# Optimization experiments

Hardware: AMD Instinct MI355X
Metric: run time of the kernel (lower is better)

Reference implementation:

```python
import jax, jax.numpy as jnp
import numpy as np
from jax import lax

RATIOS = jnp.array([0.5, 1.0, 2.0], dtype=jnp.float32)
SCALES = jnp.array([8.0, 16.0, 32.0], dtype=jnp.float32)
IOU_THR = 0.5
BATCH_SIZE = 32            # module-level constant in the source
POS_RATIO = 1.0 / 3.0      # positive_ratio in the source


def _generate_anchors(fh, fw, ih, iw):
    """Vectorized version of RPN.generate_anchors. Returns (A,4) x1y1x2y2 anchors
    and an (A,) inside-image mask (static shapes; mask replaces boolean filtering)."""
    xs = iw / fw
    ys = ih / fh
    xc = (jnp.arange(fw, dtype=jnp.float32) + 0.5) * xs
    yc = (jnp.arange(fh, dtype=jnp.float32) + 0.5) * ys
    gx, gy = jnp.meshgrid(xc, yc, indexing='ij')
    centers = jnp.stack([gx.ravel(), gy.ravel()], axis=1)          # (fh*fw, 2)
    h = jnp.sqrt(SCALES[None, :] ** 2 / RATIOS[:, None]) * ys       # (3,3)
    w = h * RATIOS[:, None] * xs / ys
    wh = jnp.stack([w.ravel(), h.ravel()], axis=1)                  # (9, 2)
    lo = centers[:, None, :] - wh[None, :, :] / 2
    hi = centers[:, None, :] + wh[None, :, :] / 2
    anchors = jnp.concatenate([lo, hi], axis=2).reshape(-1, 4)      # (A, 4)
    inside = ((anchors[:, 0] >= 0) & (anchors[:, 1] >= 0) &
              (anchors[:, 2] <= iw) & (anchors[:, 3] <= ih))
    return anchors, inside


def _iou_matrix(anchors, gts):
    """Pairwise IoU between (A,4) and (G,4) corner boxes -> (A,G). Vectorizes the
    nested python loop in the original."""
    x1 = jnp.maximum(anchors[:, None, 0], gts[None, :, 0])
    y1 = jnp.maximum(anchors[:, None, 1], gts[None, :, 1])
    x2 = jnp.minimum(anchors[:, None, 2], gts[None, :, 2])
    y2 = jnp.minimum(anchors[:, None, 3], gts[None, :, 3])
    inter = jnp.maximum(x2 - x1, 0.0) * jnp.maximum(y2 - y1, 0.0)
    area_a = (anchors[:, 2] - anchors[:, 0]) * (anchors[:, 3] - anchors[:, 1])
    area_g = (gts[:, 2] - gts[:, 0]) * (gts[:, 3] - gts[:, 1])
    union = area_a[:, None] + area_g[None, :] - inter
    return jnp.where(inter > 0, inter / union, 0.0)


def _conv(x, w, b):
    return lax.conv_general_dilated(x, w, (1, 1), 'SAME',
                                    dimension_numbers=('NHWC', 'HWIO', 'NHWC')) + b


def setup_inputs() -> dict:
    key = jax.random.key(0)
    ks = jax.random.split(key, 11)
    B, H, W, C = 8, 64, 64, 512
    IMG = 1024
    std = 0.05  # keras RandomNormal default stddev
    features = jax.random.normal(ks[0], (B, H, W, C), jnp.float32)
    # 8 rows of boxes; rows 2..7 are the object boxes used by the RPN (x1,y1,x2,y2)
    xy = jax.random.uniform(ks[1], (8, 2), jnp.float32) * (IMG * 0.7)
    wh = jax.random.uniform(ks[2], (8, 2), jnp.float32) * (IMG * 0.2) + 16.0
    ground_truths = jnp.concatenate([xy, xy + wh], axis=1)
    return {
        'features': features,
        'ground_truths': ground_truths,
        'conv1_w': jax.random.normal(ks[3], (3, 3, C, 512), jnp.float32) * std,
        'conv1_b': jnp.zeros((512,), jnp.float32),
        'reg_w': jax.random.normal(ks[4], (1, 1, 512, 72), jnp.float32) * std,
        'reg_b': jnp.zeros((72,), jnp.float32),
        'cls_w': jax.random.normal(ks[5], (1, 1, 512, 9), jnp.float32) * std,
        'cls_b': jnp.zeros((9,), jnp.float32),
        'lmk_w': jax.random.normal(ks[6], (1, 1, 512, 54), jnp.float32) * std,
        'lmk_b': jnp.zeros((54,), jnp.float32),
        'img_h': IMG,
        'img_w': IMG,
    }


def reference(features, ground_truths, conv1_w, conv1_b, reg_w, reg_b,
              cls_w, cls_b, lmk_w, lmk_b, img_h, img_w):
    B, H, W, C = features.shape
    anchors, inside = _generate_anchors(H, W, float(img_h), float(img_w))
    A = anchors.shape[0]
    gts = ground_truths[2:]                                   # (6,4)
    ious = _iou_matrix(anchors, gts)                          # (A,6)
    ious = jnp.where(inside[:, None], ious, -1.0)             # outside anchors never match

    best_iou = ious.max(axis=1)
    best_idx = ious.argmax(axis=1)
    gt_best = ious.max(axis=0)
    is_best = ((ious == gt_best[None, :]) & (gt_best[None, :] > -1.0)).any(axis=1)
    labels = jnp.where((best_iou >= IOU_THR) | is_best, 1, 0)
    labels = jnp.where(inside, labels, -1)

    # balanced subsampling (np.random.choice in the original -> rank-of-random trick)
    num_pos = int(POS_RATIO * BATCH_SIZE)
    num_neg = BATCH_SIZE - num_pos
    r = jax.random.uniform(jax.random.key(42), (A,), jnp.float32)

    def keep(mask, n):
        kv = jnp.where(mask, r, jnp.inf)
        order = jnp.argsort(kv)
        rank = jnp.zeros(A, jnp.int32).at[order].set(jnp.arange(A, dtype=jnp.int32))
        return mask & (rank < n)

    pos = keep(labels == 1, num_pos)
    neg = keep(labels == 0, num_neg)
    labels = jnp.where(pos, 1, jnp.where(neg, 0, -1)).astype(jnp.float32)

    eps = jnp.finfo(jnp.float32).eps
    wa = jnp.maximum(anchors[:, 2] - anchors[:, 0], eps)
    ha = jnp.maximum(anchors[:, 3] - anchors[:, 1], eps)
    xa = anchors[:, 0] + wa / 2
    ya = anchors[:, 1] + ha / 2
    mg = gts[best_idx]                                        # (A,4) matched gt
    wg = mg[:, 2] - mg[:, 0]
    hg = mg[:, 3] - mg[:, 1]
    xg = mg[:, 0] + wg / 2
    yg = mg[:, 1] + hg / 2
    deltas = jnp.stack([(xg - xa) / wa, (yg - ya) / ha,
                        jnp.log(wg / wa), jnp.log(hg / ha)], axis=1)
    offsets = jnp.where(pos[:, None], deltas, 0.0)            # (A,4)

    # conv heads on backbone features
    x = jax.nn.relu(_conv(features, conv1_w, conv1_b))
    anchor_deltas = _conv(x, reg_w, reg_b)                    # (B,H,W,72)
    scores = jax.nn.sigmoid(_conv(x, cls_w, cls_b))           # (B,H,W,9)
    landmarks = _conv(x, lmk_w, lmk_b)                        # (B,H,W,54)
    return anchor_deltas, scores, landmarks, labels, offsets
```

## Files before the change

### kernel.cpp

```cpp
#include <hip/hip_runtime.h>
#include <cstdint>
#include <cstddef>


#define A_TOT 36864

typedef unsigned short ushortT;
typedef __attribute__((ext_vector_type(8))) short short8;
typedef __attribute__((ext_vector_type(4))) float f32x4;

typedef __attribute__((address_space(1))) unsigned char gbyte_t;
typedef __attribute__((address_space(3))) unsigned char lbyte_t;

__device__ __forceinline__ void gld_lds16(const void* g, void* l) {
  __builtin_amdgcn_global_load_lds((gbyte_t*)g, (lbyte_t*)l, 16, 0, 0);
}

__device__ __forceinline__ uint32_t rotl32(uint32_t v, int d) { return (v << d) | (v >> (32 - d)); }

__device__ __forceinline__ ushortT f2bf(float f) {
  uint32_t u = __float_as_uint(f);
  uint32_t r = (u + 0x7FFFu + ((u >> 16) & 1u)) >> 16;
  return (ushortT)r;
}

__device__ __forceinline__ uint32_t f2mono(float f) {
  uint32_t b = __float_as_uint(f);
  return b ^ ((b >> 31) ? 0xFFFFFFFFu : 0x80000000u);
}
__device__ __forceinline__ float mono2f(uint32_t u) {
  uint32_t b = (u >> 31) ? (u ^ 0x80000000u) : ~u;
  return __uint_as_float(b);
}

__device__ uint32_t threefry_bits_for(uint32_t a) {
  uint32_t x0 = 0u, x1 = a;
  const uint32_t k0 = 0u, k1 = 42u;
  const uint32_t k2 = k0 ^ k1 ^ 0x1BD11BDAu;
  x0 += k0; x1 += k1;
#define TF_RND(r) { x0 += x1; x1 = rotl32(x1, (r)); x1 ^= x0; }
  TF_RND(13) TF_RND(15) TF_RND(26) TF_RND(6)
  x0 += k1; x1 += k2 + 1u;
  TF_RND(17) TF_RND(29) TF_RND(16) TF_RND(24)
  x0 += k2; x1 += k0 + 2u;
  TF_RND(13) TF_RND(15) TF_RND(26) TF_RND(6)
  x0 += k0; x1 += k1 + 3u;
  TF_RND(17) TF_RND(29) TF_RND(16) TF_RND(24)
  x0 += k1; x1 += k2 + 4u;
  TF_RND(13) TF_RND(15) TF_RND(26) TF_RND(6)
  x0 += k2; x1 += k0 + 5u;
#undef TF_RND
  return x0 ^ x1;
}

struct Anc { float x1, y1, x2, y2; bool inside; };

__device__ __forceinline__ Anc anchor_at(int a, float iw, float ih) {
  Anc A;
  {
    #pragma clang fp contract(off)
    int p = a / 9;
    int q = a - p * 9;
    int i = p >> 6;
    int j = p & 63;
    int ri = q / 3;
    int si = q - ri * 3;
    const float ratios[3] = {0.5f, 1.0f, 2.0f};
    const float scales[3] = {8.0f, 16.0f, 32.0f};
    float xs = iw / 64.0f;
    float ys = ih / 64.0f;
    float cx = ((float)i + 0.5f) * xs;
    float cy = ((float)j + 0.5f) * ys;
    float r = ratios[ri], s = scales[si];
    float h = sqrtf((s * s) / r) * ys;
    float w = h * r * xs / ys;
    A.x1 = cx - w * 0.5f;
    A.y1 = cy - h * 0.5f;
    A.x2 = cx + w * 0.5f;
    A.y2 = cy + h * 0.5f;
    A.inside = (A.x1 >= 0.0f) && (A.y1 >= 0.0f) && (A.x2 <= iw) && (A.y2 <= ih);
  }
  return A;
}

__device__ __forceinline__ float iou_one(const Anc& A, const float* g) {
  #pragma clang fp contract(off)
  float x1 = fmaxf(A.x1, g[0]);
  float y1 = fmaxf(A.y1, g[1]);
  float x2 = fminf(A.x2, g[2]);
  float y2 = fminf(A.y2, g[3]);
  float inter = fmaxf(x2 - x1, 0.0f) * fmaxf(y2 - y1, 0.0f);
  float area_a = (A.x2 - A.x1) * (A.y2 - A.y1);
  float area_g = (g[2] - g[0]) * (g[3] - g[1]);
  float un = (area_a + area_g) - inter;
  return inter > 0.0f ? (inter / un) : 0.0f;
}

__global__ __launch_bounds__(256) void labels_gtmax_kernel(
    const float* __restrict__ gtr, const int* __restrict__ pih, const int* __restrict__ piw,
    uint32_t* __restrict__ gtbest_bits) {
  __shared__ float s_gt[6][4];
  __shared__ float s_red[4][6];
  int tid = threadIdx.x;
  if (tid < 24) ((float*)s_gt)[tid] = gtr[8 + tid];
  __syncthreads();
  float iw = (float)piw[0], ih = (float)pih[0];
  int a = blockIdx.x * 256 + tid;
  Anc A = anchor_at(a, iw, ih);
  int w = tid >> 6;
  #pragma unroll
  for (int g = 0; g < 6; ++g) {
    float v = A.inside ? iou_one(A, s_gt[g]) : -1.0f;
    for (int off = 32; off > 0; off >>= 1) v = fmaxf(v, __shfl_down(v, off, 64));
    if ((tid & 63) == 0) s_red[w][g] = v;
  }
  __syncthreads();
  if (tid < 6) {
    float m = fmaxf(fmaxf(s_red[0][tid], s_red[1][tid]), fmaxf(s_red[2][tid], s_red[3][tid]));
    atomicMax(&gtbest_bits[tid], f2mono(m));
  }
}

__global__ __launch_bounds__(256) void labels_code_kernel(
    const float* __restrict__ gtr, const int* __restrict__ pih, const int* __restrict__ piw,
    const uint32_t* __restrict__ gtbest_bits, uint32_t* __restrict__ L) {
  __shared__ float s_gt[6][4];
  __shared__ float s_gb[6];
  int tid = threadIdx.x;
  if (tid < 24) ((float*)s_gt)[tid] = gtr[8 + tid];
  if (tid < 6) s_gb[tid] = mono2f(gtbest_bits[tid]);
  __syncthreads();
  float iw = (float)piw[0], ih = (float)pih[0];
  int a = blockIdx.x * 256 + tid;
  Anc A = anchor_at(a, iw, ih);
  uint32_t code;
  if (!A.inside) {
    code = 2u;
  } else {
    float best = -1.0f;
    bool isb = false;
    #pragma unroll
    for (int g = 0; g < 6; ++g) {
      float v = iou_one(A, s_gt[g]);
      best = fmaxf(best, v);
      if (v == s_gb[g] && s_gb[g] > -1.0f) isb = true;
    }
    code = (best >= 0.5f || isb) ? 1u : 0u;
  }
  uint32_t m = threefry_bits_for((uint32_t)a) >> 9;
  L[a] = (m << 2) | code;
}

__global__ __launch_bounds__(1024) void labels_select_kernel(
    const uint32_t* __restrict__ L, unsigned long long* __restrict__ Tsel) {
  __shared__ int hist[2][512];
  __shared__ unsigned long long list[2][512];
  __shared__ int lcnt[2];
  __shared__ int s_b[2], s_r[2];
  int tid = threadIdx.x;
  hist[tid >> 9][tid & 511] = 0;
  if (tid < 2) lcnt[tid] = 0;
  __syncthreads();
  for (int a = tid; a < A_TOT; a += 1024) {
    uint32_t v = L[a];
    uint32_t c = v & 3u;
    if (c < 2u) atomicAdd(&hist[c][v >> 16], 1);
  }
  __syncthreads();
  if (tid < 2) {
    int need = (tid == 1) ? 10 : 22;
    int tot = 0;
    for (int i = 0; i < 512; ++i) tot += hist[tid][i];
    int b = -1, r = 0, cum = 0;
    if (tot > need) {
      for (int i = 0; i < 512; ++i) {
        if (cum + hist[tid][i] >= need) { b = i; r = need - cum; break; }
        cum += hist[tid][i];
      }
    }
    s_b[tid] = b; s_r[tid] = r;
    if (b < 0) Tsel[tid] = ~0ull;
  }
  __syncthreads();
  for (int a = tid; a < A_TOT; a += 1024) {
    uint32_t v = L[a];
    uint32_t c = v & 3u;
    if (c < 2u && s_b[c] == (int)(v >> 16)) {
      int idx = atomicAdd(&lcnt[c], 1);
      if (idx < 512) list[c][idx] = (((unsigned long long)(v >> 2)) << 16) | (unsigned)a;
    }
  }
  __syncthreads();
  #pragma unroll
  for (int c = 0; c < 2; ++c) {
    if (s_b[c] < 0) continue;
    int n = lcnt[c] < 512 ? lcnt[c] : 512;
    if (tid < n) {
      unsigned long long k = list[c][tid];
      int rank = 1;
      for (int i = 0; i < n; ++i) rank += (list[c][i] < k) ? 1 : 0;
      if (rank == s_r[c]) Tsel[c] = k;
    }
  }
}

__global__ __launch_bounds__(256) void labels_final_kernel(
    const uint32_t* __restrict__ L, const unsigned long long* __restrict__ Tsel,
    const float* __restrict__ gtr, const int* __restrict__ pih, const int* __restrict__ piw,
    float* __restrict__ labels_out, float* __restrict__ offs_out) {
  __shared__ float s_gt[6][4];
  int tid = threadIdx.x;
  if (tid < 24) ((float*)s_gt)[tid] = gtr[8 + tid];
  __syncthreads();
  float iw = (float)piw[0], ih = (float)pih[0];
  int a = blockIdx.x * 256 + tid;
  uint32_t v = L[a];
  uint32_t code = v & 3u;
  unsigned long long K = (((unsigned long long)(v >> 2)) << 16) | (unsigned)a;
  bool pos = (code == 1u) && (K <= Tsel[1]);
  bool neg = (code == 0u) && (K <= Tsel[0]);
  labels_out[a] = pos ? 1.0f : (neg ? 0.0f : -1.0f);
  float o0 = 0.0f, o1 = 0.0f, o2 = 0.0f, o3 = 0.0f;
  if (pos) {
    #pragma clang fp contract(off)
    Anc A = anchor_at(a, iw, ih);
    int bi = 0;
    float bv = iou_one(A, s_gt[0]);
    for (int g = 1; g < 6; ++g) {
      float vg = iou_one(A, s_gt[g]);
      if (vg > bv) { bv = vg; bi = g; }
    }
    const float eps = 1.1920928955078125e-07f;
    float wa = fmaxf(A.x2 - A.x1, eps);
    float ha = fmaxf(A.y2 - A.y1, eps);
    float xa = A.x1 + wa * 0.5f;
    float ya = A.y1 + ha * 0.5f;
    const float* g = s_gt[bi];
    float wg = g[2] - g[0];
    float hg = g[3] - g[1];
    float xg = g[0] + wg * 0.5f;
    float yg = g[1] + hg * 0.5f;
    o0 = (xg - xa) / wa;
    o1 = (yg - ya) / ha;
    o2 = logf(wg / wa);
    o3 = logf(hg / ha);
  }
  offs_out[a * 4 + 0] = o0;
  offs_out[a * 4 + 1] = o1;
  offs_out[a * 4 + 2] = o2;
  offs_out[a * 4 + 3] = o3;
}

__global__ void prep_all_kernel(const float* __restrict__ w, const float* __restrict__ feat,
                                const float* __restrict__ reg_w, const float* __restrict__ cls_w,
                                const float* __restrict__ lmk_w, const float* __restrict__ reg_b,
                                const float* __restrict__ cls_b, const float* __restrict__ lmk_b,
                                ushortT* __restrict__ Wt, ushortT* __restrict__ featbf,
                                ushortT* __restrict__ zrow, ushortT* __restrict__ Wh,
                                float* __restrict__ bias_all, uint32_t* __restrict__ gtbest_bits,
                                int do_feat) {
  int idx = blockIdx.x * 256 + threadIdx.x;
  {
    int ic = idx & 511;
    int t = idx >> 9;
    int oc = t & 511;
    int kk = t >> 9;
    Wt[idx] = f2bf(w[((size_t)kk * 512 + ic) * 512 + oc]);
  }
  if (do_feat && idx < 2097152) {
    const float4 f0 = *(const float4*)(feat + (size_t)idx * 8);
    const float4 f1 = *(const float4*)(feat + (size_t)idx * 8 + 4);
    short8 o;
    o[0] = (short)f2bf(f0.x); o[1] = (short)f2bf(f0.y);
    o[2] = (short)f2bf(f0.z); o[3] = (short)f2bf(f0.w);
    o[4] = (short)f2bf(f1.x); o[5] = (short)f2bf(f1.y);
    o[6] = (short)f2bf(f1.z); o[7] = (short)f2bf(f1.w);
    *(short8*)(featbf + (size_t)idx * 8) = o;
  }
  if (idx < 73728) {
    int c = idx >> 9, ic = idx & 511;
    float v = 0.0f;
    if (c < 72) v = reg_w[ic * 72 + c];
    else if (c < 81) v = cls_w[ic * 9 + (c - 72)];
    else if (c < 135) v = lmk_w[ic * 54 + (c - 81)];
    Wh[idx] = f2bf(v);
  }
  if (do_feat && idx < 4096) {
    *(short8*)(zrow + (size_t)idx * 8) = (short8){0, 0, 0, 0, 0, 0, 0, 0};
  }
  if (idx < 144) {
    float bv = 0.0f;
    if (idx < 72) bv = reg_b[idx];
    else if (idx < 81) bv = cls_b[idx - 72];
    else if (idx < 135) bv = lmk_b[idx - 81];
    bias_all[idx] = bv;
  }
  if (idx < 6) gtbest_bits[idx] = f2mono(-1.0f);
}

__global__ __launch_bounds__(256) void conv3x3_mfma_kernel(
    const ushortT* __restrict__ featbf, const ushortT* __restrict__ zrow,
    const ushortT* __restrict__ Wt, const float* __restrict__ bias,
    ushortT* __restrict__ xbf) {
  __shared__ __align__(16) char smem[2][36864];
  const int tid = threadIdx.x;
  const int lane = tid & 63;
  const int w = tid >> 6;
  const int kgrp = lane >> 4;
  const int ln15 = lane & 15;
  const int wm = (w >> 1) * 64;
  const int wn = (w & 1) * 64;
  const int wn16 = wn >> 4;
  const int rowsel = wm >> 6;

  const int lin = blockIdx.x + 4 * blockIdx.y;
  const int swz = (lin & 7) * 128 + (lin >> 3);
  const int oc0 = (swz & 3) * 128;
  const int mb = swz >> 2;
  const int b = mb >> 5;
  const int y0 = (mb & 31) * 2;

  const int bn15 = lane & 15;
  const int bic = ((lane >> 4) & 3) * 8;

  f32x4 acc[4][4];
  #pragma unroll
  for (int i = 0; i < 4; ++i)
    #pragma unroll
    for (int j = 0; j < 4; ++j) acc[i][j] = (f32x4){0.f, 0.f, 0.f, 0.f};
  const short8 zv = (short8){0, 0, 0, 0, 0, 0, 0, 0};

  auto stageA = [&](int t, int bsel) {
    int ic0 = (t / 3) * 32;
    int dy = (t % 3) - 1;
    char* Ab = smem[bsel];
    #pragma unroll
    for (int i = 0; i < 2; ++i) {
      int c = w + i * 4;
      int h = c >> 2, q = c & 3;
      int ysrc = y0 + h + dy;
      bool vy = (unsigned)ysrc < 64u;
      const ushortT* rowbase = vy ? (featbf + ((size_t)((b * 64 + ysrc) * 64)) * 512) : zrow;
      const ushortT* src = rowbase + (size_t)(q * 16 + bn15) * 512 + ic0 + bic;
      gld_lds16(src, Ab + h * 6144 + 1024 + q * 1024);
    }
  };
  auto issueB = [&](int t, int bsel) {
    int ic0 = (t / 3) * 32;
    int ky = t % 3;
    char* Bb = smem[bsel] + 12288;
    #pragma unroll
    for (int i = 0; i < 6; ++i) {
      int c = w + i * 4;
      int kxr = c >> 3, cc = c & 7;
      int kk = ky * 3 + kxr;
      int n = cc * 16 + bn15;
      const ushortT* src = Wt + ((size_t)(kk * 512 + oc0 + n)) * 512 + ic0 + bic;
      gld_lds16(src, Bb + kxr * 8192 + cc * 1024);
    }
  };
  auto computeT = [&](int t, int bsel) {
    const char* Ab = smem[bsel] + rowsel * 6144;
    const char* Bb = smem[bsel] + 12288;
    int dy = (t % 3) - 1;
    int rowv = y0 + rowsel + dy;
    if ((unsigned)rowv >= 64u) return;
    #pragma unroll
    for (int kx = 0; kx < 3; ++kx) {
      const int dx = kx - 1;
      short8 bfr[4];
      #pragma unroll
      for (int j = 0; j < 4; ++j)
        bfr[j] = *(const short8*)(Bb + kx * 8192 + (wn16 + j) * 1024 + kgrp * 256 + ln15 * 16);
      short8 afr[4];
      #pragma unroll
      for (int i = 0; i < 4; ++i) {
        int xp = i * 16 + ln15 + dx + 16;
        afr[i] = *(const short8*)(Ab + (xp >> 4) * 1024 + kgrp * 256 + (xp & 15) * 16);
      }
      #pragma unroll
      for (int i = 0; i < 4; ++i)
        #pragma unroll
        for (int j = 0; j < 4; ++j)
          acc[i][j] = __builtin_amdgcn_mfma_f32_16x16x32_bf16(afr[i], bfr[j], acc[i][j], 0, 0, 0);
    }
  };

  {
    int pc = tid >> 6;
    int h = pc >> 1, side = pc & 1;
    int off = h * 6144 + side * 5120 + (tid & 63) * 16;
    *(short8*)(smem[0] + off) = zv;
    *(short8*)(smem[1] + off) = zv;
  }
  stageA(0, 0);
  issueB(0, 0);
  __syncthreads();

  int buf = 0;
  for (int t = 0; t < 48; ++t) {
    if (t < 47) { stageA(t + 1, buf ^ 1); issueB(t + 1, buf ^ 1); }
    computeT(t, buf);
    __syncthreads();
    buf ^= 1;
  }

  #pragma unroll
  for (int j = 0; j < 4; ++j) {
    int n = oc0 + wn + j * 16 + ln15;
    float bv = bias[n];
    #pragma unroll
    for (int i = 0; i < 4; ++i) {
      int mrow = mb * 128 + wm + i * 16 + kgrp * 4;
      #pragma unroll
      for (int r = 0; r < 4; ++r) {
        float v = fmaxf(acc[i][j][r] + bv, 0.0f);
        xbf[(size_t)(mrow + r) * 512 + n] = f2bf(v);
      }
    }
  }
}

__global__ __launch_bounds__(256) void conv3x3_mfma_fb_kernel(
    const float* __restrict__ feat, const ushortT* __restrict__ Wt,
    const float* __restrict__ bias, ushortT* __restrict__ xbf) {
  __shared__ __align__(16) char smem[2][32768];
  const int tid = threadIdx.x;
  const int lane = tid & 63;
  const int w = tid >> 6;
  const int kgrp = lane >> 4;
  const int ln15 = lane & 15;
  const int wm = (w >> 1) * 64;
  const int wn = (w & 1) * 64;
  const int wn16 = wn >> 4;
  const int lin = blockIdx.x + 4 * blockIdx.y;
  const int swz = (lin & 7) * 128 + (lin >> 3);
  const int oc0 = (swz & 3) * 128;
  const int mb = swz >> 2;
  const int b = mb >> 5;
  const int y0 = (mb & 31) * 2;
  const int sp0 = (tid >> 6) * 16 + (tid & 15);
  const int sk0 = ((tid >> 4) & 3) * 8;
  const int bn15 = lane & 15;
  const int bic = ((lane >> 4) & 3) * 8;

  f32x4 acc[4][4];
  #pragma unroll
  for (int i = 0; i < 4; ++i)
    #pragma unroll
    for (int j = 0; j < 4; ++j) acc[i][j] = (f32x4){0.f, 0.f, 0.f, 0.f};
  const short8 zv = (short8){0, 0, 0, 0, 0, 0, 0, 0};

  auto issueA = [&](int t, float4* aL) {
    int ic0 = (t / 3) * 32;
    int dy = (t % 3) - 1;
    #pragma unroll
    for (int h = 0; h < 2; ++h) {
      int p = sp0 + h * 64;
      int ys = y0 + (p >> 6) + dy;
      ys = ys < 0 ? 0 : (ys > 63 ? 63 : ys);
      const float* sp = feat + ((size_t)((b * 64 + ys) * 64 + (p & 63))) * 512 + ic0 + sk0;
      aL[h * 2 + 0] = *(const float4*)sp;
      aL[h * 2 + 1] = *(const float4*)(sp + 4);
    }
  };
  auto issueB = [&](int t, int bsel) {
    int ic0 = (t / 3) * 32;
    int ky = t % 3;
    char* Bb = smem[bsel] + 8192;
    #pragma unroll
    for (int i = 0; i < 6; ++i) {
      int c = w + i * 4;
      int kxr = c >> 3, cc = c & 7;
      int kk = ky * 3 + kxr;
      int n = cc * 16 + bn15;
      const ushortT* src = Wt + ((size_t)(kk * 512 + oc0 + n)) * 512 + ic0 + bic;
      gld_lds16(src, Bb + kxr * 8192 + cc * 1024);
    }
  };
  auto writeA = [&](const float4* aL, int bsel) {
    char* Ab = smem[bsel];
    #pragma unroll
    for (int h = 0; h < 2; ++h) {
      float4 f0 = aL[h * 2 + 0], f1 = aL[h * 2 + 1];
      short8 o;
      o[0] = (short)f2bf(f0.x); o[1] = (short)f2bf(f0.y);
      o[2] = (short)f2bf(f0.z); o[3] = (short)f2bf(f0.w);
      o[4] = (short)f2bf(f1.x); o[5] = (short)f2bf(f1.y);
      o[6] = (short)f2bf(f1.z); o[7] = (short)f2bf(f1.w);
      *(short8*)(Ab + h * 4096 + tid * 16) = o;
    }
  };
  auto computeT = [&](int t, int bsel) {
    const char* Ab = smem[bsel];
    const char* Bb = smem[bsel] + 8192;
    int dy = (t % 3) - 1;
    int rowv = y0 + (wm >> 6) + dy;
    if ((unsigned)rowv >= 64u) return;
    #pragma unroll
    for (int kx = 0; kx < 3; ++kx) {
      const int dx = kx - 1;
      short8 bfr[4];
      #pragma unroll
      for (int j = 0; j < 4; ++j)
        bfr[j] = *(const short8*)(Bb + kx * 8192 + (wn16 + j) * 1024 + kgrp * 256 + ln15 * 16);
      short8 afr[4];
      #pragma unroll
      for (int i = 0; i < 4; ++i) {
        int xin = i * 16 + ln15 + dx;
        bool ok = (unsigned)xin < 64u;
        int p_in = wm + (ok ? xin : 0);
        short8 v = *(const short8*)(Ab + (p_in >> 4) * 1024 + kgrp * 256 + (p_in & 15) * 16);
        afr[i] = ok ? v : zv;
      }
      #pragma unroll
      for (int i = 0; i < 4; ++i)
        #pragma unroll
        for (int j = 0; j < 4; ++j)
          acc[i][j] = __builtin_amdgcn_mfma_f32_16x16x32_bf16(afr[i], bfr[j], acc[i][j], 0, 0, 0);
    }
  };

  {
    float4 aL[4];
    issueA(0, aL);
    issueB(0, 0);
    writeA(aL, 0);
  }
  __syncthreads();

  int buf = 0;
  for (int t = 0; t < 48; ++t) {
    float4 aN[4];
    if (t < 47) { issueA(t + 1, aN); issueB(t + 1, buf ^ 1); }
    computeT(t, buf);
    if (t < 47) writeA(aN, buf ^ 1);
    __syncthreads();
    buf ^= 1;
  }

  #pragma unroll
  for (int j = 0; j < 4; ++j) {
    int n = oc0 + wn + j * 16 + ln15;
    float bv = bias[n];
    #pragma unroll
    for (int i = 0; i < 4; ++i) {
      int mrow = mb * 128 + wm + i * 16 + kgrp * 4;
      #pragma unroll
      for (int r = 0; r < 4; ++r) {
        float v = fmaxf(acc[i][j][r] + bv, 0.0f);
        xbf[(size_t)(mrow + r) * 512 + n] = f2bf(v);
      }
    }
  }
}

__global__ __launch_bounds__(256) void heads_mfma_kernel(
    const ushortT* __restrict__ x, const ushortT* __restrict__ Wh,
    const float* __restrict__ bias_all,
    float* __restrict__ out_deltas, float* __restrict__ out_scores, float* __restrict__ out_lmk) {
  __shared__ __align__(16) char smem[2][17408];
  const int tid = threadIdx.x;
  const int lane = tid & 63;
  const int w = tid >> 6;
  const int kgrp = lane >> 4;
  const int ln15 = lane & 15;
  const int m0 = blockIdx.x * 128;
  const int bn15 = lane & 15;
  const int bic = ((lane >> 4) & 3) * 8;

  f32x4 acc[2][9];
  #pragma unroll
  for (int i = 0; i < 2; ++i)
    #pragma unroll
    for (int j = 0; j < 9; ++j) acc[i][j] = (f32x4){0.f, 0.f, 0.f, 0.f};

  auto stage = [&](int t, int bsel) {
    int k0 = t * 32;
    char* Ab = smem[bsel];
    char* Bb = smem[bsel] + 8192;
    #pragma unroll
    for (int i = 0; i < 2; ++i) {
      int cc = w + i * 4;
      int p = cc * 16 + bn15;
      gld_lds16(x + ((size_t)(m0 + p)) * 512 + k0 + bic, Ab + cc * 1024);
    }
    for (int c = w; c < 9; c += 4) {
      int n = c * 16 + bn15;
      gld_lds16(Wh + ((size_t)n) * 512 + k0 + bic, Bb + c * 1024);
    }
  };
  auto computeH = [&](int bsel) {
    const char* Ab = smem[bsel];
    const char* Bb = smem[bsel] + 8192;
    short8 afr[2], bfr[9];
    #pragma unroll
    for (int i = 0; i < 2; ++i)
      afr[i] = *(const short8*)(Ab + (w * 2 + i) * 1024 + kgrp * 256 + ln15 * 16);
    #pragma unroll
    for (int j = 0; j < 9; ++j)
      bfr[j] = *(const short8*)(Bb + j * 1024 + kgrp * 256 + ln15 * 16);
    #pragma unroll
    for (int i = 0; i < 2; ++i)
      #pragma unroll
      for (int j = 0; j < 9; ++j)
        acc[i][j] = __builtin_amdgcn_mfma_f32_16x16x32_bf16(afr[i], bfr[j], acc[i][j], 0, 0, 0);
  };

  stage(0, 0);
  __syncthreads();
  int buf = 0;
  for (int t = 0; t < 16; ++t) {
    if (t < 15) stage(t + 1, buf ^ 1);
    computeH(buf);
    __syncthreads();
    buf ^= 1;
  }

  #pragma unroll
  for (int j = 0; j < 9; ++j) {
    int c = j * 16 + ln15;
    float bv = bias_all[c];
    #pragma unroll
    for (int i = 0; i < 2; ++i) {
      int mrow = m0 + w * 32 + i * 16 + kgrp * 4;
      #pragma unroll
      for (int r = 0; r < 4; ++r) {
        size_t m = (size_t)(mrow + r);
        float v = acc[i][j][r] + bv;
        if (c < 72) out_deltas[m * 72 + c] = v;
        else if (c < 81) out_scores[m * 9 + (c - 72)] = 1.0f / (1.0f + expf(-v));
        else if (c < 135) out_lmk[m * 54 + (c - 81)] = v;
      }
    }
  }
}

extern "C" void kernel_launch(void* const* d_in, const int* in_sizes, int n_in,
                              void* d_out, int out_size, void* d_ws, size_t ws_size,
                              hipStream_t stream) {
  const float* feat    = (const float*)d_in[0];
  const float* gtr     = (const float*)d_in[1];
  const float* conv1_w = (const float*)d_in[2];
  const float* conv1_b = (const float*)d_in[3];
  const float* reg_w   = (const float*)d_in[4];
  const float* reg_b   = (const float*)d_in[5];
  const float* cls_w   = (const float*)d_in[6];
  const float* cls_b   = (const float*)d_in[7];
  const float* lmk_w   = (const float*)d_in[8];
  const float* lmk_b   = (const float*)d_in[9];
  const int*   pih     = (const int*)d_in[10];
  const int*   piw     = (const int*)d_in[11];

  float* out = (float*)d_out;
  float* deltas = out;
  float* scores = out + 2359296;
  float* lmk    = out + 2654208;
  float* labels = out + 4423680;
  float* offs   = out + 4460544;

  ushortT*  Wt          = (ushortT*)d_ws;
  ushortT*  Wh          = (ushortT*)((char*)d_ws + 4718592);
  float*    bias_all    = (float*)((char*)d_ws + 4866048);
  uint32_t* gtbest_bits = (uint32_t*)((char*)d_ws + 4866688);
  unsigned long long* Tsel = (unsigned long long*)((char*)d_ws + 4866752);
  ushortT*  xbf         = (ushortT*)((char*)d_ws + 4866816);
  uint32_t* L           = (uint32_t*)((char*)d_ws + 38421248);
  ushortT*  featbf      = (ushortT*)((char*)d_ws + 38568704);
  ushortT*  zrow        = (ushortT*)((char*)d_ws + 72123136);

  const bool use_bf16A = ws_size >= 72188672ull;

  prep_all_kernel<<<9216, 256, 0, stream>>>(conv1_w, feat, reg_w, cls_w, lmk_w,
                                            reg_b, cls_b, lmk_b, Wt, featbf, zrow,
                                            Wh, bias_all, gtbest_bits,
                                            use_bf16A ? 1 : 0);

  dim3 gconv(4, 256);
  if (use_bf16A) {
    conv3x3_mfma_kernel<<<gconv, 256, 0, stream>>>(featbf, zrow, Wt, conv1_b, xbf);
  } else {
    conv3x3_mfma_fb_kernel<<<gconv, 256, 0, stream>>>(feat, Wt, conv1_b, xbf);
  }

  heads_mfma_kernel<<<256, 256, 0, stream>>>(xbf, Wh, bias_all, deltas, scores, lmk);

  labels_gtmax_kernel<<<144, 256, 0, stream>>>(gtr, pih, piw, gtbest_bits);
  labels_code_kernel<<<144, 256, 0, stream>>>(gtr, pih, piw, gtbest_bits, L);
  labels_select_kernel<<<1, 1024, 0, stream>>>(L, Tsel);
  labels_final_kernel<<<144, 256, 0, stream>>>(L, Tsel, gtr, pih, piw, labels, offs);
}
```

Before: 259.3 us.

## Split weight transpose into tiled LDS kernel and remap conv/head blocks per XCD

The fused prep kernel is split. The conv1 weight transpose moves into its own kernel, which transposes through a padded shared-memory tile so both the fp32 reads and the bf16 writes are coalesced, replacing the old strided gather. The feature cast and head-weight prep stay in a second kernel with 8192 blocks. The conv block swizzle now gives each XCD a contiguous range of 32 spatial tiles across all four output-channel groups, so the A activations are reused within one L2. The heads kernel gets a similar XCD-aware remap. The cost is one extra kernel launch.

```diff
diff --git a/kernel.cpp b/kernel.cpp
--- a/kernel.cpp
+++ b/kernel.cpp
@@ -251,23 +251,39 @@
   offs_out[a * 4 + 3] = o3;
 }
 
-__global__ void prep_all_kernel(const float* __restrict__ w, const float* __restrict__ feat,
-                                const float* __restrict__ reg_w, const float* __restrict__ cls_w,
-                                const float* __restrict__ lmk_w, const float* __restrict__ reg_b,
-                                const float* __restrict__ cls_b, const float* __restrict__ lmk_b,
-                                ushortT* __restrict__ Wt, ushortT* __restrict__ featbf,
-                                ushortT* __restrict__ zrow, ushortT* __restrict__ Wh,
-                                float* __restrict__ bias_all, uint32_t* __restrict__ gtbest_bits,
-                                int do_feat) {
+__global__ __launch_bounds__(256) void prep_wt_kernel(
+    const float* __restrict__ w, ushortT* __restrict__ Wt) {
+  __shared__ float tile[64][65];
+  int blk = blockIdx.x;
+  int kk = blk / 64;
+  int rem = blk - kk * 64;
+  int ic0 = (rem >> 3) * 64;
+  int oc0 = (rem & 7) * 64;
+  int t = threadIdx.x;
+  int tr = t >> 6;
+  int tc = t & 63;
+  #pragma unroll
+  for (int r = 0; r < 16; ++r) {
+    int ic = tr * 16 + r;
+    tile[ic][tc] = w[((size_t)(kk * 512 + ic0 + ic)) * 512 + oc0 + tc];
+  }
+  __syncthreads();
+  #pragma unroll
+  for (int r = 0; r < 16; ++r) {
+    int oc = tr * 16 + r;
+    Wt[((size_t)(kk * 512 + oc0 + oc)) * 512 + ic0 + tc] = f2bf(tile[tc][oc]);
+  }
+}
+
+__global__ void prep_misc_kernel(const float* __restrict__ feat,
+                                 const float* __restrict__ reg_w, const float* __restrict__ cls_w,
+                                 const float* __restrict__ lmk_w, const float* __restrict__ reg_b,
+                                 const float* __restrict__ cls_b, const float* __restrict__ lmk_b,
+                                 ushortT* __restrict__ featbf, ushortT* __restrict__ zrow,
+                                 ushortT* __restrict__ Wh, float* __restrict__ bias_all,
+                                 uint32_t* __restrict__ gtbest_bits, int do_feat) {
   int idx = blockIdx.x * 256 + threadIdx.x;
-  {
-    int ic = idx & 511;
-    int t = idx >> 9;
-    int oc = t & 511;
-    int kk = t >> 9;
-    Wt[idx] = f2bf(w[((size_t)kk * 512 + ic) * 512 + oc]);
-  }
-  if (do_feat && idx < 2097152) {
+  if (do_feat) {
     const float4 f0 = *(const float4*)(feat + (size_t)idx * 8);
     const float4 f1 = *(const float4*)(feat + (size_t)idx * 8 + 4);
     short8 o;
@@ -315,8 +331,10 @@
 
   const int lin = blockIdx.x + 4 * blockIdx.y;
   const int swz = (lin & 7) * 128 + (lin >> 3);
-  const int oc0 = (swz & 3) * 128;
-  const int mb = swz >> 2;
+  const int j = swz & 127;
+  const int xcd = swz >> 7;
+  const int oc0 = (j >> 5) * 128;
+  const int mb = xcd * 32 + (j & 31);
   const int b = mb >> 5;
   const int y0 = (mb & 31) * 2;
 
@@ -327,7 +345,7 @@
   #pragma unroll
   for (int i = 0; i < 4; ++i)
     #pragma unroll
-    for (int j = 0; j < 4; ++j) acc[i][j] = (f32x4){0.f, 0.f, 0.f, 0.f};
+    for (int j2 = 0; j2 < 4; ++j2) acc[i][j2] = (f32x4){0.f, 0.f, 0.f, 0.f};
   const short8 zv = (short8){0, 0, 0, 0, 0, 0, 0, 0};
 
   auto stageA = [&](int t, int bsel) {
@@ -370,8 +388,8 @@
       const int dx = kx - 1;
       short8 bfr[4];
       #pragma unroll
-      for (int j = 0; j < 4; ++j)
-        bfr[j] = *(const short8*)(Bb + kx * 8192 + (wn16 + j) * 1024 + kgrp * 256 + ln15 * 16);
+      for (int j2 = 0; j2 < 4; ++j2)
+        bfr[j2] = *(const short8*)(Bb + kx * 8192 + (wn16 + j2) * 1024 + kgrp * 256 + ln15 * 16);
       short8 afr[4];
       #pragma unroll
       for (int i = 0; i < 4; ++i) {
@@ -381,8 +399,8 @@
       #pragma unroll
       for (int i = 0; i < 4; ++i)
         #pragma unroll
-        for (int j = 0; j < 4; ++j)
-          acc[i][j] = __builtin_amdgcn_mfma_f32_16x16x32_bf16(afr[i], bfr[j], acc[i][j], 0, 0, 0);
+        for (int j2 = 0; j2 < 4; ++j2)
+          acc[i][j2] = __builtin_amdgcn_mfma_f32_16x16x32_bf16(afr[i], bfr[j2], acc[i][j2], 0, 0, 0);
     }
   };
 
@@ -406,15 +424,15 @@
   }
 
   #pragma unroll
-  for (int j = 0; j < 4; ++j) {
-    int n = oc0 + wn + j * 16 + ln15;
+  for (int j2 = 0; j2 < 4; ++j2) {
+    int n = oc0 + wn + j2 * 16 + ln15;
     float bv = bias[n];
     #pragma unroll
     for (int i = 0; i < 4; ++i) {
       int mrow = mb * 128 + wm + i * 16 + kgrp * 4;
       #pragma unroll
       for (int r = 0; r < 4; ++r) {
-        float v = fmaxf(acc[i][j][r] + bv, 0.0f);
+        float v = fmaxf(acc[i][j2][r] + bv, 0.0f);
         xbf[(size_t)(mrow + r) * 512 + n] = f2bf(v);
       }
     }
@@ -565,7 +583,9 @@
   const int w = tid >> 6;
   const int kgrp = lane >> 4;
   const int ln15 = lane & 15;
-  const int m0 = blockIdx.x * 128;
+  const int lin = blockIdx.x;
+  const int swz = (lin & 7) * 32 + (lin >> 3);
+  const int m0 = swz * 128;
   const int bn15 = lane & 15;
   const int bic = ((lane >> 4) & 3) * 8;
 
@@ -671,10 +691,11 @@
 
   const bool use_bf16A = ws_size >= 72188672ull;
 
-  prep_all_kernel<<<9216, 256, 0, stream>>>(conv1_w, feat, reg_w, cls_w, lmk_w,
-                                            reg_b, cls_b, lmk_b, Wt, featbf, zrow,
-                                            Wh, bias_all, gtbest_bits,
-                                            use_bf16A ? 1 : 0);
+  prep_wt_kernel<<<576, 256, 0, stream>>>(conv1_w, Wt);
+  prep_misc_kernel<<<8192, 256, 0, stream>>>(feat, reg_w, cls_w, lmk_w,
+                                             reg_b, cls_b, lmk_b, featbf, zrow,
+                                             Wh, bias_all, gtbest_bits,
+                                             use_bf16A ? 1 : 0);
 
   dim3 gconv(4, 256);
   if (use_bf16A) {
```

Result: no change. 257.9 us (-0.5%).
